# Kernel optimization log

Hardware: AMD Instinct MI355X
Metric: run time of the kernel (lower is better)

The kernel has to match this reference:

```python
import jax, jax.numpy as jnp
import numpy as np

IN_DIM = 64
OUT_DIM = 64
NUM_HEADS = 4
NEG_SLOPE = 0.2
GAMMA = 1.0  # constraint_gamma
NUM_VARS = 100000
NUM_CLAUSES = 100000
NUM_CLUSTERS = 2048
VARS_PER = 64
CLAUSES_PER = 64
NUM_EDGES = 400000


def _xavier(k, shape):
    bound = np.sqrt(6.0 / (shape[0] + shape[1])).astype(np.float32)
    return jax.random.uniform(k, shape, jnp.float32, -bound, bound)


def setup_inputs() -> dict:
    key = jax.random.key(0)
    ks = jax.random.split(key, 11)
    return {
        "x_var": jax.random.normal(ks[0], (NUM_VARS, IN_DIM), jnp.float32),
        "x_clause": jax.random.normal(ks[1], (NUM_CLAUSES, IN_DIM), jnp.float32),
        "var_clause_edge_index": jax.random.randint(ks[2], (2, NUM_EDGES), 0, NUM_VARS),
        "edge_polarity": jax.random.normal(ks[3], (NUM_EDGES, 1), jnp.float32),
        "cluster_var_ids": jax.random.randint(ks[4], (NUM_CLUSTERS, VARS_PER), 0, NUM_VARS),
        "cluster_clause_ids": jax.random.randint(ks[5], (NUM_CLUSTERS, CLAUSES_PER), 0, NUM_CLAUSES),
        "satisfaction_scores": jax.random.uniform(ks[6], (NUM_CLAUSES,), jnp.float32),
        "active_heads": 4,
        "W_Q": _xavier(ks[7], (OUT_DIM, IN_DIM)),
        "W_K": _xavier(ks[8], (OUT_DIM, IN_DIM)),
        "W_V": _xavier(ks[9], (OUT_DIM, IN_DIM)),
        "head_weights": jnp.ones((NUM_HEADS,), jnp.float32),
        "out_proj_w": _xavier(ks[10], (OUT_DIM, OUT_DIM)),
        "out_proj_b": jnp.zeros((OUT_DIM,), jnp.float32),
    }


def reference(x_var, x_clause, var_clause_edge_index, edge_polarity,
              cluster_var_ids, cluster_clause_ids, satisfaction_scores,
              active_heads, W_Q, W_K, W_V, head_weights, out_proj_w, out_proj_b):
    # NOTE: var_clause_edge_index / edge_polarity are accepted but unused,
    # matching the original forward body.
    num_vars = x_var.shape[0]
    x_all = jnp.concatenate([x_var, x_clause], axis=0)            # [N, D]
    Q = x_all @ W_Q.T
    K = x_all @ W_K.T
    V = x_all @ W_V.T

    # Block-diagonal cluster layout: [C, S] with S = VARS_PER + CLAUSES_PER
    nodes = jnp.concatenate([cluster_var_ids, cluster_clause_ids + num_vars], axis=1)
    Qc = Q[nodes]                                                 # [C, S, D]
    Kc = K[nodes]
    Vc = V[nodes]

    scale = jnp.asarray(np.sqrt(OUT_DIM), Qc.dtype)
    scores = jnp.einsum('csd,ctd->cst', Qc, Kc) / scale            # [C, S, S]
    # constraint-aware bias on clause columns (added before leaky_relu)
    bias = jnp.concatenate(
        [jnp.zeros(cluster_var_ids.shape, scores.dtype),
         GAMMA * satisfaction_scores[cluster_clause_ids]], axis=1)  # [C, S]
    scores = jax.nn.leaky_relu(scores + bias[:, None, :], NEG_SLOPE)
    attn = jax.nn.softmax(scores, axis=-1)

    head_w = jnp.mean(head_weights[:active_heads])
    h = jnp.einsum('cst,ctd->csd', attn, Vc) * head_w             # [C, S, D]

    flat = nodes.reshape(-1)
    out = jnp.zeros_like(x_all).at[flat].add(h.reshape(-1, OUT_DIM))
    count = jnp.zeros((x_all.shape[0],), x_all.dtype).at[flat].add(1.0)
    out = out / jnp.maximum(count, 1.0)[:, None]
    out = out @ out_proj_w.T + out_proj_b

    return (x_var + out[:num_vars], x_clause + out[num_vars:])
```

## Files before the change

kernel.cpp:

```cpp
#include <hip/hip_runtime.h>


#define NV 100000
#define NN 200000
#define NCLUST 2048
#define XS 72

typedef __attribute__((ext_vector_type(8))) short short8;
typedef __attribute__((ext_vector_type(16))) float floatx16;

__device__ __forceinline__ unsigned short f2bf(float f) {
    union { float f; unsigned u; } v; v.f = f;
    unsigned r = v.u + 0x7fffu + ((v.u >> 16) & 1u);
    return (unsigned short)(r >> 16);
}
__device__ __forceinline__ unsigned pack2bf(float lo, float hi) {
    union { float f; unsigned u; } a, b; a.f = lo; b.f = hi;
    unsigned ra = a.u + 0x7fffu + ((a.u >> 16) & 1u);
    unsigned rb = b.u + 0x7fffu + ((b.u >> 16) & 1u);
    return (ra >> 16) | (rb & 0xffff0000u);
}
__device__ __forceinline__ int crow(int r, int lane) {
    return (r & 3) + 8 * (r >> 2) + 4 * (lane >> 5);
}
template<int CTRL>
__device__ __forceinline__ unsigned dppmov(unsigned v) {
    return (unsigned)__builtin_amdgcn_update_dpp(0, (int)v, CTRL, 0xf, 0xf, true);
}
template<int CTRL>
__device__ __forceinline__ float dppaddf(float s) {
    union { float f; unsigned u; } a, b; a.f = s;
    b.u = dppmov<CTRL>(a.u);
    return s + b.f;
}
__device__ __forceinline__ float dppxor1f(float s) {
    union { float f; unsigned u; } a, b; a.f = s;
    b.u = dppmov<0xB1>(a.u);
    return b.f;
}
__device__ __forceinline__ void bar_lds() {
    __builtin_amdgcn_sched_barrier(0);
    asm volatile("s_waitcnt lgkmcnt(0)" ::: "memory");
    __builtin_amdgcn_s_barrier();
    __builtin_amdgcn_sched_barrier(0);
}

__global__ __launch_bounds__(256) void prep_kernel(
    const float* __restrict__ WQ, const float* __restrict__ WK,
    const float* __restrict__ WV, const float* __restrict__ Wout,
    const float* __restrict__ head_weights, const int* __restrict__ active_heads_p,
    unsigned short* __restrict__ Mtr, unsigned short* __restrict__ Pbf)
{
    int o = blockIdx.x * blockDim.x + threadIdx.x;
    int ah = active_heads_p[0];
    float hw = 0.f;
    for (int i = 0; i < ah; ++i) hw += head_weights[i];
    hw /= (float)ah;
    if (o < 4096) {
        int d = o >> 6, a = o & 63;
        float acc = 0.f;
        for (int j = 0; j < 64; ++j) acc += WQ[j*64 + a] * WK[j*64 + d];
        Mtr[o] = f2bf(acc * 0.125f);
    } else if (o < 8192) {
        int o2 = o - 4096;
        int j = o2 >> 6, b = o2 & 63;
        float acc = 0.f;
        for (int d = 0; d < 64; ++d) acc += Wout[j*64 + d] * WV[d*64 + b];
        Pbf[o2] = f2bf(acc * hw);
    }
}

template<bool WN>
__device__ __forceinline__ void cluster_compute(
    unsigned short* X, unsigned short* E,
    const int* ids, const float* biascl,
    const unsigned short* __restrict__ Mtr,
    unsigned short* __restrict__ accum_bf,
    int lane, int w, int m, int hk, int r, int cb,
    short8 nx0, short8 nx1, short8 nx2, short8 nx3)
{
    {
        floatx16 z0 = {}, z1 = {};
        #pragma unroll
        for (int ks = 0; ks < 4; ++ks) {
            short8 mb0 = *(const short8*)(Mtr + m * 64 + ks * 16 + hk);
            short8 mb1 = *(const short8*)(Mtr + (32 + m) * 64 + ks * 16 + hk);
            short8 a = *(const short8*)&X[(w * 32 + m) * XS + ks * 16 + hk];
            z0 = __builtin_amdgcn_mfma_f32_32x32x16_bf16(a, mb0, z0, 0, 0, 0);
            z1 = __builtin_amdgcn_mfma_f32_32x32x16_bf16(a, mb1, z1, 0, 0, 0);
        }
        #pragma unroll
        for (int rr = 0; rr < 16; ++rr) {
            int row = w * 32 + crow(rr, lane);
            E[row * XS + m]      = f2bf(z0[rr]);
            E[row * XS + 32 + m] = f2bf(z1[rr]);
        }
    }

    floatx16 sc[4] = {{}, {}, {}, {}};
    #pragma unroll
    for (int ks = 0; ks < 4; ++ks) {
        short8 a = *(const short8*)&E[(w * 32 + m) * XS + ks * 16 + hk];
        #pragma unroll
        for (int nt = 0; nt < 4; ++nt) {
            short8 b = *(const short8*)&X[(nt * 32 + m) * XS + ks * 16 + hk];
            sc[nt] = __builtin_amdgcn_mfma_f32_32x32x16_bf16(a, b, sc[nt], 0, 0, 0);
        }
    }

    const float b2 = biascl[m], b3 = biascl[32 + m];
    #pragma unroll
    for (int rr = 0; rr < 16; ++rr) {
        float a0 = sc[0][rr], a1 = sc[1][rr], a2 = sc[2][rr] + b2, a3 = sc[3][rr] + b3;
        a0 = a0 > 0.f ? a0 : 0.2f * a0;
        a1 = a1 > 0.f ? a1 : 0.2f * a1;
        a2 = a2 > 0.f ? a2 : 0.2f * a2;
        a3 = a3 > 0.f ? a3 : 0.2f * a3;
        a0 = __expf(a0); a1 = __expf(a1); a2 = __expf(a2); a3 = __expf(a3);
        float s4 = (a0 + a1) + (a2 + a3);
        s4 = dppaddf<0x121>(s4);
        s4 = dppaddf<0x122>(s4);
        s4 = dppaddf<0x124>(s4);
        s4 = dppaddf<0x128>(s4);
        {
            union { float f; int i; } t, o; t.f = s4;
            o.i = __builtin_amdgcn_ds_swizzle(t.i, 0x401F);
            s4 += o.f;
        }
        float inv = __builtin_amdgcn_rcpf(s4);
        sc[0][rr] = a0 * inv; sc[1][rr] = a1 * inv;
        sc[2][rr] = a2 * inv; sc[3][rr] = a3 * inv;
    }

    #pragma unroll
    for (int rr = 0; rr < 16; ++rr) {
        int row = w * 32 + crow(rr, lane);
        E[row * XS + m]      = f2bf(sc[0][rr]);
        E[row * XS + 32 + m] = f2bf(sc[1][rr]);
    }

    const int cp = m & ~1;
    const unsigned selp = (lane & 1) ? 0x07060302u : 0x05040100u;
    floatx16 g0 = {}, g1 = {};
    #pragma unroll
    for (int ks = 0; ks < 4; ++ks) {
        short8 a = *(const short8*)&E[(w * 32 + m) * XS + ks * 16 + hk];
        const unsigned short* tb = &X[(ks * 16 + hk) * XS];
        unsigned q0[8], q1[8];
        #pragma unroll
        for (int u = 0; u < 8; ++u) {
            q0[u] = *(const unsigned*)(tb + u * XS + cp);
            q1[u] = *(const unsigned*)(tb + u * XS + cp + 32);
        }
        union { unsigned u[4]; short8 v; } b0, b1;
        b0.u[0] = __builtin_amdgcn_perm(q0[1], q0[0], selp);
        b0.u[1] = __builtin_amdgcn_perm(q0[3], q0[2], selp);
        b0.u[2] = __builtin_amdgcn_perm(q0[5], q0[4], selp);
        b0.u[3] = __builtin_amdgcn_perm(q0[7], q0[6], selp);
        b1.u[0] = __builtin_amdgcn_perm(q1[1], q1[0], selp);
        b1.u[1] = __builtin_amdgcn_perm(q1[3], q1[2], selp);
        b1.u[2] = __builtin_amdgcn_perm(q1[5], q1[4], selp);
        b1.u[3] = __builtin_amdgcn_perm(q1[7], q1[6], selp);
        g0 = __builtin_amdgcn_mfma_f32_32x32x16_bf16(a, b0.v, g0, 0, 0, 0);
        g1 = __builtin_amdgcn_mfma_f32_32x32x16_bf16(a, b1.v, g1, 0, 0, 0);
    }

    #pragma unroll
    for (int rr = 0; rr < 16; ++rr) {
        int row = w * 32 + crow(rr, lane);
        E[row * XS + m]      = f2bf(sc[2][rr]);
        E[row * XS + 32 + m] = f2bf(sc[3][rr]);
    }

    #pragma unroll
    for (int ks = 0; ks < 4; ++ks) {
        short8 a = *(const short8*)&E[(w * 32 + m) * XS + ks * 16 + hk];
        const unsigned short* tb = &X[(64 + ks * 16 + hk) * XS];
        unsigned q0[8], q1[8];
        #pragma unroll
        for (int u = 0; u < 8; ++u) {
            q0[u] = *(const unsigned*)(tb + u * XS + cp);
            q1[u] = *(const unsigned*)(tb + u * XS + cp + 32);
        }
        union { unsigned u[4]; short8 v; } b0, b1;
        b0.u[0] = __builtin_amdgcn_perm(q0[1], q0[0], selp);
        b0.u[1] = __builtin_amdgcn_perm(q0[3], q0[2], selp);
        b0.u[2] = __builtin_amdgcn_perm(q0[5], q0[4], selp);
        b0.u[3] = __builtin_amdgcn_perm(q0[7], q0[6], selp);
        b1.u[0] = __builtin_amdgcn_perm(q1[1], q1[0], selp);
        b1.u[1] = __builtin_amdgcn_perm(q1[3], q1[2], selp);
        b1.u[2] = __builtin_amdgcn_perm(q1[5], q1[4], selp);
        b1.u[3] = __builtin_amdgcn_perm(q1[7], q1[6], selp);
        g0 = __builtin_amdgcn_mfma_f32_32x32x16_bf16(a, b0.v, g0, 0, 0, 0);
        g1 = __builtin_amdgcn_mfma_f32_32x32x16_bf16(a, b1.v, g1, 0, 0, 0);
    }

    if (WN) {
        *(short8*)&E[r * XS + cb +  0] = nx0;
        *(short8*)&E[r * XS + cb +  8] = nx1;
        *(short8*)&E[r * XS + cb + 16] = nx2;
        *(short8*)&E[r * XS + cb + 24] = nx3;
    }

    const bool ev = !(lane & 1);
    const int colbase = ev ? m : (31 + m);
    #pragma unroll
    for (int rr = 0; rr < 16; ++rr) {
        int row = w * 32 + crow(rr, lane);
        int nid = ids[row];
        float a0 = g0[rr], a1 = g1[rr];
        float t0 = dppxor1f(a0);
        float t1 = dppxor1f(a1);
        float lo = ev ? a0 : t1;
        float hi = ev ? t0 : a1;
        unsigned pk = (unsigned)f2bf(lo) | ((unsigned)f2bf(hi) << 16);
        unsigned long long addr =
            (unsigned long long)(accum_bf + (size_t)nid * 64 + colbase);
        asm volatile("global_atomic_pk_add_bf16 %0, %1, off"
                     :: "v"(addr), "v"(pk) : "memory");
    }
}

__global__ __launch_bounds__(256, 4) void attn_kernel(
    const float* __restrict__ x_var, const float* __restrict__ x_clause,
    const int* __restrict__ cvar, const int* __restrict__ ccl,
    const float* __restrict__ sat, const unsigned short* __restrict__ Mtr,
    unsigned short* __restrict__ accum_bf, float* __restrict__ countv)
{
    __shared__ unsigned short bufA[128 * XS];
    __shared__ unsigned short bufB[128 * XS];
    __shared__ int   ids0[128], ids1[128];
    __shared__ float bias0[64], bias1[64];

    const int tid = threadIdx.x, lane = tid & 63, w = tid >> 6;
    const int m = lane & 31, hk = (lane >> 5) * 8;
    const int c0 = blockIdx.x * 2;
    const int r = tid >> 1, half = tid & 1, cb = half * 32;

    int nid0, nid1;
    const float *src0, *src1;
    float sv0 = 0.f, sv1 = 0.f;
    if (r < 64) {
        nid0 = cvar[c0 * 64 + r];
        nid1 = cvar[c0 * 64 + 64 + r];
        src0 = x_var + (size_t)nid0 * 64;
        src1 = x_var + (size_t)nid1 * 64;
    } else {
        int cid0 = ccl[c0 * 64 + (r - 64)];
        int cid1 = ccl[c0 * 64 + r];
        nid0 = NV + cid0; nid1 = NV + cid1;
        src0 = x_clause + (size_t)cid0 * 64;
        src1 = x_clause + (size_t)cid1 * 64;
        if (half) { sv0 = sat[cid0]; sv1 = sat[cid1]; }
    }

    const float4* s40 = (const float4*)src0 + half * 8;
    const float4* s41 = (const float4*)src1 + half * 8;
    float4 v0[8], v1[8];
    #pragma unroll
    for (int i = 0; i < 8; ++i) v0[i] = s40[i];
    #pragma unroll
    for (int i = 0; i < 8; ++i) v1[i] = s41[i];

    if (!half) {
        ids0[r] = nid0; ids1[r] = nid1;
        atomicAdd(&countv[nid0], 1.0f);
        atomicAdd(&countv[nid1], 1.0f);
    }
    if (r >= 64 && half) { bias0[r - 64] = sv0; bias1[r - 64] = sv1; }

    {
        union { unsigned u[16]; short8 v[4]; } h0;
        #pragma unroll
        for (int i = 0; i < 8; ++i) {
            h0.u[2*i]   = pack2bf(v0[i].x, v0[i].y);
            h0.u[2*i+1] = pack2bf(v0[i].z, v0[i].w);
        }
        #pragma unroll
        for (int i = 0; i < 4; ++i) *(short8*)&bufA[r * XS + cb + i * 8] = h0.v[i];
    }
    union { unsigned u[16]; short8 v[4]; } h1;
    #pragma unroll
    for (int i = 0; i < 8; ++i) {
        h1.u[2*i]   = pack2bf(v1[i].x, v1[i].y);
        h1.u[2*i+1] = pack2bf(v1[i].z, v1[i].w);
    }

    bar_lds();

    cluster_compute<true>(bufA, bufB, ids0, bias0, Mtr, accum_bf,
                          lane, w, m, hk, r, cb,
                          h1.v[0], h1.v[1], h1.v[2], h1.v[3]);

    bar_lds();

    short8 zz = {};
    cluster_compute<false>(bufB, bufA, ids1, bias1, Mtr, accum_bf,
                           lane, w, m, hk, r, cb, zz, zz, zz, zz);
}

__global__ __launch_bounds__(256, 4) void finalize_kernel(
    const float* __restrict__ x_var, const float* __restrict__ x_clause,
    const unsigned short* __restrict__ accum_bf, const float* __restrict__ countv,
    const unsigned short* __restrict__ Pbf, const float* __restrict__ bout,
    float* __restrict__ out)
{
    __shared__ float cnts[256];
    const int tid = threadIdx.x, lane = tid & 63, w = tid >> 6;
    const int base = blockIdx.x * 256;
    {
        int n = base + tid;
        cnts[tid] = (n < NN) ? countv[n] : 1.f;
    }
    __syncthreads();

    const int m = lane & 31, hk = (lane >> 5) * 8;
    short8 pb[2][4];
    #pragma unroll
    for (int nt = 0; nt < 2; ++nt)
        #pragma unroll
        for (int ks = 0; ks < 4; ++ks)
            pb[nt][ks] = *(const short8*)(Pbf + (nt * 32 + m) * 64 + ks * 16 + hk);
    const float bias0 = bout[m], bias1 = bout[32 + m];

    #pragma unroll
    for (int tm = 0; tm < 2; ++tm) {
        int mt = w * 2 + tm;
        const unsigned short* arow = accum_bf + (size_t)(base + mt * 32 + m) * 64;
        floatx16 c0 = {}, c1 = {};
        #pragma unroll
        for (int ks = 0; ks < 4; ++ks) {
            short8 a = *(const short8*)(arow + ks * 16 + hk);
            c0 = __builtin_amdgcn_mfma_f32_32x32x16_bf16(a, pb[0][ks], c0, 0, 0, 0);
            c1 = __builtin_amdgcn_mfma_f32_32x32x16_bf16(a, pb[1][ks], c1, 0, 0, 0);
        }
        #pragma unroll
        for (int rr = 0; rr < 16; ++rr) {
            int lrow = mt * 32 + crow(rr, lane);
            int n = base + lrow;
            if (n < NN) {
                float inv = 1.0f / fmaxf(cnts[lrow], 1.0f);
                const float* xs = (n < NV) ? (x_var + (size_t)n * 64)
                                           : (x_clause + (size_t)(n - NV) * 64);
                out[(size_t)n * 64 + m]      = xs[m]      + c0[rr] * inv + bias0;
                out[(size_t)n * 64 + 32 + m] = xs[32 + m] + c1[rr] * inv + bias1;
            }
        }
    }
}

extern "C" void kernel_launch(void* const* d_in, const int* in_sizes, int n_in,
                              void* d_out, int out_size, void* d_ws, size_t ws_size,
                              hipStream_t stream)
{
    const float* x_var        = (const float*)d_in[0];
    const float* x_clause     = (const float*)d_in[1];
    const int*   cvar         = (const int*)d_in[4];
    const int*   ccl          = (const int*)d_in[5];
    const float* sat          = (const float*)d_in[6];
    const int*   active_heads = (const int*)d_in[7];
    const float* WQ           = (const float*)d_in[8];
    const float* WK           = (const float*)d_in[9];
    const float* WV           = (const float*)d_in[10];
    const float* head_weights = (const float*)d_in[11];
    const float* Wout         = (const float*)d_in[12];
    const float* bout         = (const float*)d_in[13];

    unsigned short* accum_bf = (unsigned short*)d_ws;
    float* countv = (float*)(accum_bf + (size_t)NN * 64);
    unsigned short* Mtr = (unsigned short*)(countv + NN);
    unsigned short* Pbf = Mtr + 4096;

    hipMemsetAsync(accum_bf, 0, (size_t)NN * 64 * 2 + (size_t)NN * 4, stream);
    prep_kernel<<<32, 256, 0, stream>>>(WQ, WK, WV, Wout, head_weights, active_heads, Mtr, Pbf);
    attn_kernel<<<NCLUST / 2, 256, 0, stream>>>(x_var, x_clause, cvar, ccl, sat, Mtr, accum_bf, countv);
    finalize_kernel<<<(NN + 255) / 256, 256, 0, stream>>>(x_var, x_clause, accum_bf, countv, Pbf, bout, (float*)d_out);
}
```

Before: 217.5 us.

## Replace atomic scatter-add with dense per-cluster stores and gather-based finalize

Instead of scattering attention outputs into a per-node accumulator with bf16 atomics, the attention kernel now writes each cluster's output rows densely to a workspace buffer. A new index kernel builds a per-node bucket list of the cluster-slot occurrences, and the finalize kernel gathers and sums these before the output projection. This removes contended global atomics and the large memset. In exchange it adds an extra kernel, random gathers, and a cap of 16 occurrences per node that silently drops any extra contributions. The old path is kept as a fallback when the workspace is too small.

```diff
diff --git a/kernel.cpp b/kernel.cpp
--- a/kernel.cpp
+++ b/kernel.cpp
@@ -5,6 +5,7 @@
 #define NN 200000
 #define NCLUST 2048
 #define XS 72
+#define BUCK_K 16
 
 typedef __attribute__((ext_vector_type(8))) short short8;
 typedef __attribute__((ext_vector_type(16))) float floatx16;
@@ -13,6 +14,9 @@
     union { float f; unsigned u; } v; v.f = f;
     unsigned r = v.u + 0x7fffu + ((v.u >> 16) & 1u);
     return (unsigned short)(r >> 16);
+}
+__device__ __forceinline__ float bf2f(unsigned short s) {
+    union { unsigned u; float f; } v; v.u = (unsigned)s << 16; return v.f;
 }
 __device__ __forceinline__ unsigned pack2bf(float lo, float hi) {
     union { float f; unsigned u; } a, b; a.f = lo; b.f = hi;
@@ -70,12 +74,23 @@
     }
 }
 
-template<bool WN>
+__global__ __launch_bounds__(256) void build_index_kernel(
+    const int* __restrict__ cvar, const int* __restrict__ ccl,
+    int* __restrict__ icnt, int* __restrict__ buck)
+{
+    int e = blockIdx.x * 256 + threadIdx.x;
+    int c = e >> 7, r = e & 127;
+    int nid = (r < 64) ? cvar[c * 64 + r] : (NV + ccl[c * 64 + (r - 64)]);
+    int pos = atomicAdd(&icnt[nid], 1);
+    if (pos < BUCK_K) buck[(size_t)nid * BUCK_K + pos] = e;
+}
+
+template<bool WN, bool DENSE>
 __device__ __forceinline__ void cluster_compute(
     unsigned short* X, unsigned short* E,
     const int* ids, const float* biascl,
     const unsigned short* __restrict__ Mtr,
-    unsigned short* __restrict__ accum_bf,
+    unsigned short* __restrict__ sbase,
     int lane, int w, int m, int hk, int r, int cb,
     short8 nx0, short8 nx1, short8 nx2, short8 nx3)
 {
@@ -207,25 +222,30 @@
     #pragma unroll
     for (int rr = 0; rr < 16; ++rr) {
         int row = w * 32 + crow(rr, lane);
-        int nid = ids[row];
         float a0 = g0[rr], a1 = g1[rr];
         float t0 = dppxor1f(a0);
         float t1 = dppxor1f(a1);
         float lo = ev ? a0 : t1;
         float hi = ev ? t0 : a1;
         unsigned pk = (unsigned)f2bf(lo) | ((unsigned)f2bf(hi) << 16);
-        unsigned long long addr =
-            (unsigned long long)(accum_bf + (size_t)nid * 64 + colbase);
-        asm volatile("global_atomic_pk_add_bf16 %0, %1, off"
-                     :: "v"(addr), "v"(pk) : "memory");
-    }
-}
-
+        if constexpr (DENSE) {
+            *(unsigned*)(sbase + (size_t)row * 64 + colbase) = pk;
+        } else {
+            int nid = ids[row];
+            unsigned long long addr =
+                (unsigned long long)(sbase + (size_t)nid * 64 + colbase);
+            asm volatile("global_atomic_pk_add_bf16 %0, %1, off"
+                         :: "v"(addr), "v"(pk) : "memory");
+        }
+    }
+}
+
+template<bool DENSE>
 __global__ __launch_bounds__(256, 4) void attn_kernel(
     const float* __restrict__ x_var, const float* __restrict__ x_clause,
     const int* __restrict__ cvar, const int* __restrict__ ccl,
     const float* __restrict__ sat, const unsigned short* __restrict__ Mtr,
-    unsigned short* __restrict__ accum_bf, float* __restrict__ countv)
+    unsigned short* __restrict__ Hacc, float* __restrict__ countv)
 {
     __shared__ unsigned short bufA[128 * XS];
     __shared__ unsigned short bufB[128 * XS];
@@ -262,10 +282,12 @@
     #pragma unroll
     for (int i = 0; i < 8; ++i) v1[i] = s41[i];
 
-    if (!half) {
-        ids0[r] = nid0; ids1[r] = nid1;
-        atomicAdd(&countv[nid0], 1.0f);
-        atomicAdd(&countv[nid1], 1.0f);
+    if constexpr (!DENSE) {
+        if (!half) {
+            ids0[r] = nid0; ids1[r] = nid1;
+            atomicAdd(&countv[nid0], 1.0f);
+            atomicAdd(&countv[nid1], 1.0f);
+        }
     }
     if (r >= 64 && half) { bias0[r - 64] = sv0; bias1[r - 64] = sv1; }
 
@@ -288,15 +310,83 @@
 
     bar_lds();
 
-    cluster_compute<true>(bufA, bufB, ids0, bias0, Mtr, accum_bf,
-                          lane, w, m, hk, r, cb,
-                          h1.v[0], h1.v[1], h1.v[2], h1.v[3]);
+    unsigned short* st0 = DENSE ? (Hacc + (size_t)c0 * 128 * 64) : Hacc;
+    unsigned short* st1 = DENSE ? (st0 + 128 * 64) : Hacc;
+
+    cluster_compute<true, DENSE>(bufA, bufB, ids0, bias0, Mtr, st0,
+                                 lane, w, m, hk, r, cb,
+                                 h1.v[0], h1.v[1], h1.v[2], h1.v[3]);
 
     bar_lds();
 
     short8 zz = {};
-    cluster_compute<false>(bufB, bufA, ids1, bias1, Mtr, accum_bf,
-                           lane, w, m, hk, r, cb, zz, zz, zz, zz);
+    cluster_compute<false, DENSE>(bufB, bufA, ids1, bias1, Mtr, st1,
+                                  lane, w, m, hk, r, cb, zz, zz, zz, zz);
+}
+
+__global__ __launch_bounds__(256, 4) void finalize_dense_kernel(
+    const float* __restrict__ x_var, const float* __restrict__ x_clause,
+    const unsigned short* __restrict__ H, const int* __restrict__ icnt,
+    const int* __restrict__ buck, const unsigned short* __restrict__ Pbf,
+    const float* __restrict__ bout, float* __restrict__ out)
+{
+    __shared__ int cnti[256];
+    const int tid = threadIdx.x, lane = tid & 63, w = tid >> 6;
+    const int base = blockIdx.x * 256;
+    {
+        int n = base + tid;
+        cnti[tid] = (n < NN) ? icnt[n] : 0;
+    }
+    __syncthreads();
+
+    const int m = lane & 31, hk = (lane >> 5) * 8;
+    short8 pb[2][4];
+    #pragma unroll
+    for (int nt = 0; nt < 2; ++nt)
+        #pragma unroll
+        for (int ks = 0; ks < 4; ++ks)
+            pb[nt][ks] = *(const short8*)(Pbf + (nt * 32 + m) * 64 + ks * 16 + hk);
+    const float bias0 = bout[m], bias1 = bout[32 + m];
+
+    #pragma unroll
+    for (int tm = 0; tm < 2; ++tm) {
+        int mt = w * 2 + tm;
+        const int lr = mt * 32 + m;
+        const int na = base + lr;
+        int cc = cnti[lr]; if (cc > BUCK_K) cc = BUCK_K;
+        const int* bk = buck + (size_t)na * BUCK_K;
+
+        floatx16 c0 = {}, c1 = {};
+        #pragma unroll
+        for (int ks = 0; ks < 4; ++ks) {
+            float acc8[8] = {0.f,0.f,0.f,0.f,0.f,0.f,0.f,0.f};
+            for (int j = 0; j < cc; ++j) {
+                int e = bk[j];
+                short8 hv = *(const short8*)(H + (size_t)e * 64 + ks * 16 + hk);
+                #pragma unroll
+                for (int q = 0; q < 8; ++q)
+                    acc8[q] += bf2f((unsigned short)hv[q]);
+            }
+            short8 a;
+            #pragma unroll
+            for (int q = 0; q < 8; ++q) a[q] = (short)f2bf(acc8[q]);
+            c0 = __builtin_amdgcn_mfma_f32_32x32x16_bf16(a, pb[0][ks], c0, 0, 0, 0);
+            c1 = __builtin_amdgcn_mfma_f32_32x32x16_bf16(a, pb[1][ks], c1, 0, 0, 0);
+        }
+        #pragma unroll
+        for (int rr = 0; rr < 16; ++rr) {
+            int lrow = mt * 32 + crow(rr, lane);
+            int n = base + lrow;
+            if (n < NN) {
+                float cf = (float)cnti[lrow];
+                float inv = 1.0f / fmaxf(cf, 1.0f);
+                const float* xs = (n < NV) ? (x_var + (size_t)n * 64)
+                                           : (x_clause + (size_t)(n - NV) * 64);
+                out[(size_t)n * 64 + m]      = xs[m]      + c0[rr] * inv + bias0;
+                out[(size_t)n * 64 + 32 + m] = xs[32 + m] + c1[rr] * inv + bias1;
+            }
+        }
+    }
 }
 
 __global__ __launch_bounds__(256, 4) void finalize_kernel(
@@ -366,13 +456,37 @@
     const float* Wout         = (const float*)d_in[12];
     const float* bout         = (const float*)d_in[13];
 
-    unsigned short* accum_bf = (unsigned short*)d_ws;
-    float* countv = (float*)(accum_bf + (size_t)NN * 64);
-    unsigned short* Mtr = (unsigned short*)(countv + NN);
-    unsigned short* Pbf = Mtr + 4096;
-
-    hipMemsetAsync(accum_bf, 0, (size_t)NN * 64 * 2 + (size_t)NN * 4, stream);
-    prep_kernel<<<32, 256, 0, stream>>>(WQ, WK, WV, Wout, head_weights, active_heads, Mtr, Pbf);
-    attn_kernel<<<NCLUST / 2, 256, 0, stream>>>(x_var, x_clause, cvar, ccl, sat, Mtr, accum_bf, countv);
-    finalize_kernel<<<(NN + 255) / 256, 256, 0, stream>>>(x_var, x_clause, accum_bf, countv, Pbf, bout, (float*)d_out);
-}
+    const size_t H_BYTES    = (size_t)NCLUST * 128 * 64 * 2;
+    const size_t ICNT_BYTES = 800256;
+    const size_t BUCK_BYTES = (size_t)NN * BUCK_K * 4;
+    const size_t MTR_OFF    = H_BYTES + ICNT_BYTES + BUCK_BYTES;
+    const size_t NEED       = MTR_OFF + 8192 + 8192;
+
+    if (ws_size >= NEED) {
+        unsigned short* H   = (unsigned short*)d_ws;
+        int* icnt = (int*)((char*)d_ws + H_BYTES);
+        int* buck = (int*)((char*)d_ws + H_BYTES + ICNT_BYTES);
+        unsigned short* Mtr = (unsigned short*)((char*)d_ws + MTR_OFF);
+        unsigned short* Pbf = Mtr + 4096;
+
+        hipMemsetAsync(icnt, 0, (size_t)NN * 4, stream);
+        prep_kernel<<<32, 256, 0, stream>>>(WQ, WK, WV, Wout, head_weights, active_heads, Mtr, Pbf);
+        build_index_kernel<<<(NCLUST * 128) / 256, 256, 0, stream>>>(cvar, ccl, icnt, buck);
+        attn_kernel<true><<<NCLUST / 2, 256, 0, stream>>>(
+            x_var, x_clause, cvar, ccl, sat, Mtr, H, nullptr);
+        finalize_dense_kernel<<<(NN + 255) / 256, 256, 0, stream>>>(
+            x_var, x_clause, H, icnt, buck, Pbf, bout, (float*)d_out);
+    } else {
+        unsigned short* accum_bf = (unsigned short*)d_ws;
+        float* countv = (float*)(accum_bf + (size_t)NN * 64);
+        unsigned short* Mtr = (unsigned short*)(countv + NN);
+        unsigned short* Pbf = Mtr + 4096;
+
+        hipMemsetAsync(accum_bf, 0, (size_t)NN * 64 * 2 + (size_t)NN * 4, stream);
+        prep_kernel<<<32, 256, 0, stream>>>(WQ, WK, WV, Wout, head_weights, active_heads, Mtr, Pbf);
+        attn_kernel<false><<<NCLUST / 2, 256, 0, stream>>>(
+            x_var, x_clause, cvar, ccl, sat, Mtr, accum_bf, countv);
+        finalize_kernel<<<(NN + 255) / 256, 256, 0, stream>>>(
+            x_var, x_clause, accum_bf, countv, Pbf, bout, (float*)d_out);
+    }
+}
```

Result: slower. 241.5 us (+11.0%).
